# Optimization experiments

Measured on AMD Instinct MI355X. Metric: run time of the kernel, lower is better.

The kernel has to match this reference:

```python
import jax, jax.numpy as jnp
import numpy as np


def setup_inputs() -> dict:
    key = jax.random.key(0)
    k1, k2 = jax.random.split(key)
    inputs = jax.random.normal(k1, (32768, 512), dtype=jnp.float32)
    codebook = jax.random.normal(k2, (8192, 512), dtype=jnp.float32)
    return {"inputs": inputs, "codebook": codebook}


def reference(inputs, codebook):
    # inputs: [N, D] (flattened), codebook: [K, D]
    D = codebook.shape[1]
    x = inputs.reshape(-1, D)                          # [N, D]
    cb_sqr = jnp.sum(codebook ** 2, axis=1)            # [K]
    x_sqr = jnp.sum(x ** 2, axis=1, keepdims=True)     # [N, 1]
    distances = (cb_sqr[None, :] + x_sqr) - 2.0 * jnp.einsum('nd,kd->nk', x, codebook)
    soft_distances = jax.nn.softmax(-distances, axis=1)  # [N, K]
    return soft_distances
```

## Files before the change

### kernel.cpp

```cpp
#include <hip/hip_runtime.h>


typedef __attribute__((ext_vector_type(8))) __bf16 bf16x8;
typedef __attribute__((ext_vector_type(4))) float f32x4;

typedef __attribute__((address_space(1))) const void global_cvoid;
typedef __attribute__((address_space(3))) void lds_void;

__device__ inline unsigned short f32_to_bf16_rne(float f) {
    unsigned int u = __float_as_uint(f);
    unsigned int r = u + 0x7FFFu + ((u >> 16) & 1u);
    return (unsigned short)(r >> 16);
}
__device__ inline float bf16u_to_f32(unsigned short h) {
    return __uint_as_float(((unsigned int)h) << 16);
}

__global__ void split_kernel(const float* __restrict__ in,
                             unsigned short* __restrict__ hi,
                             unsigned short* __restrict__ lo, int n4) {
    int i = blockIdx.x * blockDim.x + threadIdx.x;
    int stride = gridDim.x * blockDim.x;
    for (; i < n4; i += stride) {
        float4 v = reinterpret_cast<const float4*>(in)[i];
        float vv[4] = {v.x, v.y, v.z, v.w};
        ushort4 hv, lv;
        unsigned short h[4], l[4];
#pragma unroll
        for (int j = 0; j < 4; ++j) {
            h[j] = f32_to_bf16_rne(vv[j]);
            float r = vv[j] - bf16u_to_f32(h[j]);
            l[j] = f32_to_bf16_rne(r);
        }
        hv.x = h[0]; hv.y = h[1]; hv.z = h[2]; hv.w = h[3];
        lv.x = l[0]; lv.y = l[1]; lv.z = l[2]; lv.w = l[3];
        reinterpret_cast<ushort4*>(hi)[i] = hv;
        reinterpret_cast<ushort4*>(lo)[i] = lv;
    }
}

__global__ void rowsq_kernel(const float* __restrict__ cb, float* __restrict__ out) {
    int row = blockIdx.x * 4 + (threadIdx.x >> 6);
    int lane = threadIdx.x & 63;
    const float4* p = reinterpret_cast<const float4*>(cb + (size_t)row * 512);
    float4 a = p[lane];
    float4 b = p[lane + 64];
    float s = a.x * a.x + a.y * a.y + a.z * a.z + a.w * a.w +
              b.x * b.x + b.y * b.y + b.z * b.z + b.w * b.w;
#pragma unroll
    for (int o = 32; o >= 1; o >>= 1) s += __shfl_xor(s, o);
    if (lane == 0) out[row] = s;
}


#define RD_A(mq_, kk_, b_)                                                        \
    { _Pragma("unroll") for (int m = 0; m < 4; ++m) {                             \
        int r_ = wm * 128 + ((mq_) * 4 + m) * 16 + fr;                            \
        int sl_ = r_ * 4 + (fg ^ ((r_ >> 2) & 3));                                \
        afr[m] = *(const bf16x8*)&lds[b_][0][kk_][sl_ * 8];                       \
    } }

#define RD_B(kk_, b_)                                                             \
    { _Pragma("unroll") for (int n = 0; n < 4; ++n) {                             \
        int r_ = wn * 64 + n * 16 + fr;                                           \
        int sl_ = r_ * 4 + (fg ^ ((r_ >> 2) & 3));                                \
        bfr[n] = *(const bf16x8*)&lds[b_][1][kk_][sl_ * 8];                       \
    } }

#define ST(mat_, kk_, b_, tt_)                                                    \
    { int prod_ = (tt_) >> 3, ch_ = (tt_) & 7;                                    \
      const unsigned short* bse_;                                                 \
      if ((mat_) == 0) bse_ = (prod_ < 2 ? Ah : Al) + arow0;                      \
      else             bse_ = (prod_ == 1 ? Bl : Bh) + brow0;                     \
      bse_ += ch_ * 64 + (kk_) * 32;                                              \
      _Pragma("unroll") for (int j = 0; j < 2; ++j)                               \
          __builtin_amdgcn_global_load_lds((global_cvoid*)(bse_ + goff[j]),       \
              (lds_void*)&lds[b_][mat_][kk_][sl8[j]], 16, 0, 0);                  \
    }

#define MM(mq_)                                                                   \
    { _Pragma("unroll") for (int m = 0; m < 4; ++m)                               \
      _Pragma("unroll") for (int n = 0; n < 4; ++n)                               \
          acc[(mq_) * 4 + m][n] = __builtin_amdgcn_mfma_f32_16x16x32_bf16(        \
              afr[m], bfr[n], acc[(mq_) * 4 + m][n], 0, 0, 0); }

#define MID()                                                                     \
    { __builtin_amdgcn_s_barrier();                                               \
      asm volatile("s_waitcnt lgkmcnt(0)" ::: "memory");                          \
      __builtin_amdgcn_sched_barrier(0); }

#define CLOSEP()                                                                  \
    { __builtin_amdgcn_sched_barrier(0);                                          \
      __builtin_amdgcn_s_barrier();                                               \
      __builtin_amdgcn_sched_barrier(0); }

#define CLOSEV4()                                                                 \
    { asm volatile("s_waitcnt vmcnt(4)" ::: "memory");                            \
      __builtin_amdgcn_sched_barrier(0);                                          \
      __builtin_amdgcn_s_barrier();                                               \
      __builtin_amdgcn_sched_barrier(0); }

#define CLOSEV0()                                                                 \
    { asm volatile("s_waitcnt vmcnt(0)" ::: "memory");                            \
      __builtin_amdgcn_sched_barrier(0);                                          \
      __builtin_amdgcn_s_barrier();                                               \
      __builtin_amdgcn_sched_barrier(0); }

template <int F16>
__global__ __launch_bounds__(512, 2) void gemm_kernel(
    const unsigned short* __restrict__ Ah, const unsigned short* __restrict__ Al,
    const unsigned short* __restrict__ Bh, const unsigned short* __restrict__ Bl,
    const float* __restrict__ cbq, float* __restrict__ outf,
    unsigned short* __restrict__ p16, float* __restrict__ max_part,
    float* __restrict__ sum_part) {
    __shared__ __align__(16) unsigned short lds[2][2][2][8192];

    const int t = threadIdx.x;
    const int lane = t & 63;
    const int w = t >> 6;
    const int wm = w >> 2, wn = w & 3;
    const int fr = lane & 15, fg = lane >> 4;

    int bid = blockIdx.x;
    int swz = (bid & 7) * 512 + (bid >> 3);
    const int bm = swz >> 5, bn = swz & 31;
    const int row0 = bm * 256, col0 = bn * 256;
    const size_t arow0 = (size_t)row0 * 512;
    const size_t brow0 = (size_t)col0 * 512;

    int goff[2], sl8[2];
#pragma unroll
    for (int j = 0; j < 2; ++j) {
        int s = j * 512 + t;
        int r_ = s >> 2, cp_ = s & 3;
        int cl_ = cp_ ^ ((r_ >> 2) & 3);
        goff[j] = r_ * 512 + cl_ * 8;
        sl8[j] = s * 8;
    }

    f32x4 acc[8][4] = {};
    bf16x8 afr[4], bfr[4];

    ST(0, 0, 0, 0);
    ST(1, 0, 0, 0);
    ST(0, 1, 0, 0);
    ST(1, 1, 0, 0);
    CLOSEV4();

    for (int tt = 0; tt < 23; ++tt) {
        const int cb = tt & 1, nb = cb ^ 1;
        RD_A(0, 0, cb); RD_B(0, cb);
        ST(0, 0, nb, tt + 1);
        MID();
        __builtin_amdgcn_s_setprio(1); MM(0); __builtin_amdgcn_s_setprio(0);
        CLOSEP();
        RD_A(1, 0, cb);
        ST(1, 0, nb, tt + 1);
        MID();
        __builtin_amdgcn_s_setprio(1); MM(1); __builtin_amdgcn_s_setprio(0);
        CLOSEV4();
        RD_A(0, 1, cb); RD_B(1, cb);
        ST(0, 1, nb, tt + 1);
        MID();
        __builtin_amdgcn_s_setprio(1); MM(0); __builtin_amdgcn_s_setprio(0);
        CLOSEP();
        RD_A(1, 1, cb);
        ST(1, 1, nb, tt + 1);
        MID();
        __builtin_amdgcn_s_setprio(1); MM(1); __builtin_amdgcn_s_setprio(0);
        CLOSEV4();
    }
    {
        RD_A(0, 0, 1); RD_B(0, 1);
        MID();
        __builtin_amdgcn_s_setprio(1); MM(0); __builtin_amdgcn_s_setprio(0);
        CLOSEP();
        RD_A(1, 0, 1);
        MID();
        __builtin_amdgcn_s_setprio(1); MM(1); __builtin_amdgcn_s_setprio(0);
        CLOSEV0();
        RD_A(0, 1, 1); RD_B(1, 1);
        MID();
        __builtin_amdgcn_s_setprio(1); MM(0); __builtin_amdgcn_s_setprio(0);
        CLOSEP();
        RD_A(1, 1, 1);
        MID();
        __builtin_amdgcn_s_setprio(1); MM(1); __builtin_amdgcn_s_setprio(0);
        CLOSEP();
    }

    float* redm = (float*)&lds[0][0][0][0];
    float* reds = redm + 1024;

    float cq[4];
#pragma unroll
    for (int n = 0; n < 4; ++n) cq[n] = cbq[col0 + wn * 64 + n * 16 + fr];
#pragma unroll
    for (int m = 0; m < 8; ++m)
#pragma unroll
        for (int n = 0; n < 4; ++n)
#pragma unroll
            for (int r = 0; r < 4; ++r)
                acc[m][n][r] = 2.0f * acc[m][n][r] - cq[n];

    float rmx[8][4];
#pragma unroll
    for (int m = 0; m < 8; ++m)
#pragma unroll
        for (int r = 0; r < 4; ++r) {
            float v = fmaxf(fmaxf(acc[m][0][r], acc[m][1][r]),
                            fmaxf(acc[m][2][r], acc[m][3][r]));
#pragma unroll
            for (int o = 1; o < 16; o <<= 1) v = fmaxf(v, __shfl_xor(v, o));
            rmx[m][r] = v;
        }
    if (fr == 0) {
#pragma unroll
        for (int m = 0; m < 8; ++m)
#pragma unroll
            for (int r = 0; r < 4; ++r)
                redm[wn * 256 + wm * 128 + m * 16 + fg * 4 + r] = rmx[m][r];
    }
    __syncthreads();
#pragma unroll
    for (int m = 0; m < 8; ++m)
#pragma unroll
        for (int r = 0; r < 4; ++r) {
            int row = wm * 128 + m * 16 + fg * 4 + r;
            rmx[m][r] = fmaxf(fmaxf(redm[row], redm[256 + row]),
                              fmaxf(redm[512 + row], redm[768 + row]));
        }
#pragma unroll
    for (int m = 0; m < 8; ++m)
#pragma unroll
        for (int r = 0; r < 4; ++r) {
            float s = 0.f;
#pragma unroll
            for (int n = 0; n < 4; ++n) s += __expf(acc[m][n][r] - rmx[m][r]);
#pragma unroll
            for (int o = 1; o < 16; o <<= 1) s += __shfl_xor(s, o);
            if (fr == 0) reds[wn * 256 + wm * 128 + m * 16 + fg * 4 + r] = s;
        }
    __syncthreads();
    if (wn == 0 && fr == 0) {
#pragma unroll
        for (int m = 0; m < 8; ++m)
#pragma unroll
            for (int r = 0; r < 4; ++r) {
                int row = wm * 128 + m * 16 + fg * 4 + r;
                size_t gr = (size_t)(row0 + row);
                max_part[gr * 32 + bn] = rmx[m][r];
                sum_part[gr * 32 + bn] =
                    reds[row] + reds[256 + row] + reds[512 + row] + reds[768 + row];
            }
    }
#pragma unroll
    for (int m = 0; m < 8; ++m)
#pragma unroll
        for (int n = 0; n < 4; ++n)
#pragma unroll
            for (int r = 0; r < 4; ++r) {
                size_t gr = (size_t)(row0 + wm * 128 + m * 16 + fg * 4 + r);
                size_t gi = gr * 8192 + col0 + wn * 64 + n * 16 + fr;
                if constexpr (F16) {
                    union { _Float16 h; unsigned short u; } cv;
                    cv.h = (_Float16)__expf(acc[m][n][r] - rmx[m][r]);
                    p16[gi] = cv.u;
                } else {
                    outf[gi] = acc[m][n][r];
                }
            }
}

__global__ void combine_kernel(const float* __restrict__ max_part,
                               const float* __restrict__ sum_part,
                               float* __restrict__ row_m, float* __restrict__ row_is,
                               float* __restrict__ scale, int do_scale) {
    int row = blockIdx.x * 8 + (threadIdx.x >> 5);
    int l = threadIdx.x & 31;
    size_t off = (size_t)row * 32 + l;
    float m = max_part[off];
    float s = sum_part[off];
    float gm = m;
#pragma unroll
    for (int o = 16; o >= 1; o >>= 1) gm = fmaxf(gm, __shfl_xor(gm, o, 32));
    float c = s * __expf(m - gm);
#pragma unroll
    for (int o = 16; o >= 1; o >>= 1) c += __shfl_xor(c, o, 32);
    float inv = 1.0f / c;
    if (do_scale) scale[off] = __expf(m - gm) * inv;
    if (l == 0) {
        row_m[row] = gm;
        row_is[row] = inv;
    }
}

__global__ void norm_kernel(float* __restrict__ out, const float* __restrict__ row_m,
                            const float* __restrict__ row_is) {
    size_t i = (size_t)blockIdx.x * blockDim.x + threadIdx.x;
    size_t stride = (size_t)gridDim.x * blockDim.x;
    const size_t n4 = 268435456ull / 4;
    float4* p = reinterpret_cast<float4*>(out);
    for (; i < n4; i += stride) {
        int row = (int)(i >> 11);
        float m = row_m[row];
        float is = row_is[row];
        float4 v = p[i];
        v.x = __expf(v.x - m) * is;
        v.y = __expf(v.y - m) * is;
        v.z = __expf(v.z - m) * is;
        v.w = __expf(v.w - m) * is;
        p[i] = v;
    }
}

__global__ void norm_f16_kernel(const unsigned short* __restrict__ p16,
                                const float* __restrict__ scale,
                                float* __restrict__ out) {
    size_t i = (size_t)blockIdx.x * blockDim.x + threadIdx.x;
    size_t stride = (size_t)gridDim.x * blockDim.x;
    const size_t ng = 268435456ull / 8;
    const uint4* src = reinterpret_cast<const uint4*>(p16);
    float4* dst = reinterpret_cast<float4*>(out);
    for (; i < ng; i += stride) {
        int row = (int)(i >> 10);
        int bn = (int)((i >> 5) & 31);
        float s = scale[(size_t)row * 32 + bn];
        union { uint4 u; _Float16 h[8]; } cv;
        cv.u = src[i];
        float4 o1, o2;
        o1.x = (float)cv.h[0] * s; o1.y = (float)cv.h[1] * s;
        o1.z = (float)cv.h[2] * s; o1.w = (float)cv.h[3] * s;
        o2.x = (float)cv.h[4] * s; o2.y = (float)cv.h[5] * s;
        o2.z = (float)cv.h[6] * s; o2.w = (float)cv.h[7] * s;
        dst[i * 2] = o1;
        dst[i * 2 + 1] = o2;
    }
}

extern "C" void kernel_launch(void* const* d_in, const int* in_sizes, int n_in,
                              void* d_out, int out_size, void* d_ws, size_t ws_size,
                              hipStream_t stream) {
    const float* x = (const float*)d_in[0];
    const float* cb = (const float*)d_in[1];
    float* out = (float*)d_out;
    char* ws = (char*)d_ws;

    unsigned short* Xh = (unsigned short*)(ws);
    unsigned short* Xl = (unsigned short*)(ws + 33554432ull);
    unsigned short* Ch = (unsigned short*)(ws + 67108864ull);
    unsigned short* Cl = (unsigned short*)(ws + 75497472ull);
    float* cbq       = (float*)(ws + 83886080ull);
    float* max_part  = (float*)(ws + 83918848ull);
    float* sum_part  = (float*)(ws + 88113152ull);
    float* row_m     = (float*)(ws + 92307456ull);
    float* row_is    = (float*)(ws + 92438528ull);
    float* scale     = (float*)(ws + 92569600ull);
    unsigned short* p16 = (unsigned short*)(ws + 96763904ull);

    const bool f16path = (ws_size >= 633634816ull);

    split_kernel<<<2048, 256, 0, stream>>>(x, Xh, Xl, 32768 * 512 / 4);
    split_kernel<<<1024, 256, 0, stream>>>(cb, Ch, Cl, 8192 * 512 / 4);
    rowsq_kernel<<<2048, 256, 0, stream>>>(cb, cbq);
    if (f16path) {
        gemm_kernel<1><<<4096, 512, 0, stream>>>(Xh, Xl, Ch, Cl, cbq, out, p16,
                                                 max_part, sum_part);
        combine_kernel<<<4096, 256, 0, stream>>>(max_part, sum_part, row_m, row_is,
                                                 scale, 1);
        norm_f16_kernel<<<4096, 256, 0, stream>>>(p16, scale, out);
    } else {
        gemm_kernel<0><<<4096, 512, 0, stream>>>(Xh, Xl, Ch, Cl, cbq, out, p16,
                                                 max_part, sum_part);
        combine_kernel<<<4096, 256, 0, stream>>>(max_part, sum_part, row_m, row_is,
                                                 scale, 0);
        norm_kernel<<<4096, 256, 0, stream>>>(out, row_m, row_is);
    }
}
```

Baseline: 1.407 ms.

## Replace fine-grained interleaved GEMM pipeline with simple per-tile double buffering

```diff
diff --git a/kernel.cpp b/kernel.cpp
--- a/kernel.cpp
+++ b/kernel.cpp
@@ -53,58 +53,17 @@
 }
 
 
-#define RD_A(mq_, kk_, b_)                                                        \
-    { _Pragma("unroll") for (int m = 0; m < 4; ++m) {                             \
-        int r_ = wm * 128 + ((mq_) * 4 + m) * 16 + fr;                            \
-        int sl_ = r_ * 4 + (fg ^ ((r_ >> 2) & 3));                                \
-        afr[m] = *(const bf16x8*)&lds[b_][0][kk_][sl_ * 8];                       \
-    } }
-
-#define RD_B(kk_, b_)                                                             \
-    { _Pragma("unroll") for (int n = 0; n < 4; ++n) {                             \
-        int r_ = wn * 64 + n * 16 + fr;                                           \
-        int sl_ = r_ * 4 + (fg ^ ((r_ >> 2) & 3));                                \
-        bfr[n] = *(const bf16x8*)&lds[b_][1][kk_][sl_ * 8];                       \
-    } }
-
-#define ST(mat_, kk_, b_, tt_)                                                    \
-    { int prod_ = (tt_) >> 3, ch_ = (tt_) & 7;                                    \
-      const unsigned short* bse_;                                                 \
-      if ((mat_) == 0) bse_ = (prod_ < 2 ? Ah : Al) + arow0;                      \
-      else             bse_ = (prod_ == 1 ? Bl : Bh) + brow0;                     \
-      bse_ += ch_ * 64 + (kk_) * 32;                                              \
-      _Pragma("unroll") for (int j = 0; j < 2; ++j)                               \
-          __builtin_amdgcn_global_load_lds((global_cvoid*)(bse_ + goff[j]),       \
-              (lds_void*)&lds[b_][mat_][kk_][sl8[j]], 16, 0, 0);                  \
-    }
-
-#define MM(mq_)                                                                   \
-    { _Pragma("unroll") for (int m = 0; m < 4; ++m)                               \
-      _Pragma("unroll") for (int n = 0; n < 4; ++n)                               \
-          acc[(mq_) * 4 + m][n] = __builtin_amdgcn_mfma_f32_16x16x32_bf16(        \
-              afr[m], bfr[n], acc[(mq_) * 4 + m][n], 0, 0, 0); }
-
-#define MID()                                                                     \
-    { __builtin_amdgcn_s_barrier();                                               \
-      asm volatile("s_waitcnt lgkmcnt(0)" ::: "memory");                          \
-      __builtin_amdgcn_sched_barrier(0); }
-
-#define CLOSEP()                                                                  \
-    { __builtin_amdgcn_sched_barrier(0);                                          \
-      __builtin_amdgcn_s_barrier();                                               \
-      __builtin_amdgcn_sched_barrier(0); }
-
-#define CLOSEV4()                                                                 \
-    { asm volatile("s_waitcnt vmcnt(4)" ::: "memory");                            \
-      __builtin_amdgcn_sched_barrier(0);                                          \
-      __builtin_amdgcn_s_barrier();                                               \
-      __builtin_amdgcn_sched_barrier(0); }
-
-#define CLOSEV0()                                                                 \
-    { asm volatile("s_waitcnt vmcnt(0)" ::: "memory");                            \
-      __builtin_amdgcn_sched_barrier(0);                                          \
-      __builtin_amdgcn_s_barrier();                                               \
-      __builtin_amdgcn_sched_barrier(0); }
+#define ST_ALL(tt_, b_)                                                                 \
+    { int prod_ = (tt_) >> 3, ch_ = (tt_) & 7;                                          \
+      const unsigned short* Abase_ = (prod_ < 2 ? Ah : Al) + arow0 + ch_ * 64;          \
+      const unsigned short* Bbase_ = (prod_ == 1 ? Bl : Bh) + brow0 + ch_ * 64;         \
+      _Pragma("unroll") for (int kk_ = 0; kk_ < 2; ++kk_) {                             \
+        _Pragma("unroll") for (int j = 0; j < 2; ++j) {                                 \
+          __builtin_amdgcn_global_load_lds((global_cvoid*)(Abase_ + kk_ * 32 + goff[j]),\
+              (lds_void*)&lds[b_][0][kk_][sl8[j]], 16, 0, 0);                           \
+          __builtin_amdgcn_global_load_lds((global_cvoid*)(Bbase_ + kk_ * 32 + goff[j]),\
+              (lds_void*)&lds[b_][1][kk_][sl8[j]], 16, 0, 0);                           \
+        } } }
 
 template <int F16>
 __global__ __launch_bounds__(512, 2) void gemm_kernel(
@@ -128,6 +87,10 @@
     const size_t arow0 = (size_t)row0 * 512;
     const size_t brow0 = (size_t)col0 * 512;
 
+    const int xsl = fg ^ ((fr >> 2) & 3);
+    const int a_slot = (wm * 128 + fr) * 4 + xsl;
+    const int b_slot = (wn * 64 + fr) * 4 + xsl;
+
     int goff[2], sl8[2];
 #pragma unroll
     for (int j = 0; j < 2; ++j) {
@@ -139,54 +102,48 @@
     }
 
     f32x4 acc[8][4] = {};
-    bf16x8 afr[4], bfr[4];
-
-    ST(0, 0, 0, 0);
-    ST(1, 0, 0, 0);
-    ST(0, 1, 0, 0);
-    ST(1, 1, 0, 0);
-    CLOSEV4();
-
-    for (int tt = 0; tt < 23; ++tt) {
-        const int cb = tt & 1, nb = cb ^ 1;
-        RD_A(0, 0, cb); RD_B(0, cb);
-        ST(0, 0, nb, tt + 1);
-        MID();
-        __builtin_amdgcn_s_setprio(1); MM(0); __builtin_amdgcn_s_setprio(0);
-        CLOSEP();
-        RD_A(1, 0, cb);
-        ST(1, 0, nb, tt + 1);
-        MID();
-        __builtin_amdgcn_s_setprio(1); MM(1); __builtin_amdgcn_s_setprio(0);
-        CLOSEV4();
-        RD_A(0, 1, cb); RD_B(1, cb);
-        ST(0, 1, nb, tt + 1);
-        MID();
-        __builtin_amdgcn_s_setprio(1); MM(0); __builtin_amdgcn_s_setprio(0);
-        CLOSEP();
-        RD_A(1, 1, cb);
-        ST(1, 1, nb, tt + 1);
-        MID();
-        __builtin_amdgcn_s_setprio(1); MM(1); __builtin_amdgcn_s_setprio(0);
-        CLOSEV4();
-    }
-    {
-        RD_A(0, 0, 1); RD_B(0, 1);
-        MID();
-        __builtin_amdgcn_s_setprio(1); MM(0); __builtin_amdgcn_s_setprio(0);
-        CLOSEP();
-        RD_A(1, 0, 1);
-        MID();
-        __builtin_amdgcn_s_setprio(1); MM(1); __builtin_amdgcn_s_setprio(0);
-        CLOSEV0();
-        RD_A(0, 1, 1); RD_B(1, 1);
-        MID();
-        __builtin_amdgcn_s_setprio(1); MM(0); __builtin_amdgcn_s_setprio(0);
-        CLOSEP();
-        RD_A(1, 1, 1);
-        MID();
-        __builtin_amdgcn_s_setprio(1); MM(1); __builtin_amdgcn_s_setprio(0);
-        CLOSEP();
+
+    ST_ALL(0, 0);
+
+    for (int tt = 0; tt < 24; ++tt) {
+        const int cur = tt & 1;
+        __builtin_amdgcn_sched_barrier(0);
+        __builtin_amdgcn_s_barrier();
+        __builtin_amdgcn_sched_barrier(0);
+        if (tt < 23) {
+            ST_ALL(tt + 1, cur ^ 1);
+            asm volatile("s_waitcnt vmcnt(8)" ::: "memory");
+        } else {
+            asm volatile("s_waitcnt vmcnt(0)" ::: "memory");
+        }
+        __builtin_amdgcn_sched_barrier(0);
+        __builtin_amdgcn_s_barrier();
+        __builtin_amdgcn_sched_barrier(0);
+#pragma unroll
+        for (int kk = 0; kk < 2; ++kk) {
+            bf16x8 bfr[4], afrA[4], afrB[4];
+#pragma unroll
+            for (int n = 0; n < 4; ++n)
+                bfr[n] = *(const bf16x8*)&lds[cur][1][kk][(b_slot + n * 64) * 8];
+#pragma unroll
+            for (int m = 0; m < 4; ++m)
+                afrA[m] = *(const bf16x8*)&lds[cur][0][kk][(a_slot + m * 64) * 8];
+#pragma unroll
+            for (int m = 0; m < 4; ++m)
+                afrB[m] = *(const bf16x8*)&lds[cur][0][kk][(a_slot + (m + 4) * 64) * 8];
+#pragma unroll
+            for (int m = 0; m < 4; ++m)
+#pragma unroll
+                for (int n = 0; n < 4; ++n)
+                    acc[m][n] = __builtin_amdgcn_mfma_f32_16x16x32_bf16(
+                        afrA[m], bfr[n], acc[m][n], 0, 0, 0);
+#pragma unroll
+            for (int m = 0; m < 4; ++m)
+#pragma unroll
+                for (int n = 0; n < 4; ++n)
+                    acc[4 + m][n] = __builtin_amdgcn_mfma_f32_16x16x32_bf16(
+                        afrB[m], bfr[n], acc[4 + m][n], 0, 0, 0);
+        }
     }
 
     float* redm = (float*)&lds[0][0][0][0];
@@ -214,6 +171,7 @@
             for (int o = 1; o < 16; o <<= 1) v = fmaxf(v, __shfl_xor(v, o));
             rmx[m][r] = v;
         }
+    __syncthreads();
     if (fr == 0) {
 #pragma unroll
         for (int m = 0; m < 8; ++m)
```

Measured after the change: 1.602 ms. 13.9% more time.
